# Optimization experiments

Hardware: AMD Instinct MI355X
Metric: run time of the kernel (lower is better)

## Reference

```python
import jax, jax.numpy as jnp
import numpy as np

NEG = float(-2**32 + 1)
LN_EPS = 1e-5

def setup_inputs() -> dict:
    key = jax.random.key(0)
    ks = jax.random.split(key, 10)
    B, Sq, Sk, D = 8, 1024, 1024, 1024
    memory = jax.random.normal(ks[0], (B, Sk, D), jnp.float32)
    decoder_input = jax.random.normal(ks[1], (B, Sq, D), jnp.float32)
    query_mask = jax.random.uniform(ks[2], (B, Sq), jnp.float32)
    Wk = jax.random.normal(ks[3], (D, D), jnp.float32) * 0.02
    Wv = jax.random.normal(ks[4], (D, D), jnp.float32) * 0.02
    Wq = jax.random.normal(ks[5], (D, D), jnp.float32) * 0.02
    Wf = jax.random.normal(ks[6], (2 * D, D), jnp.float32) * 0.02
    bf = jnp.zeros((D,), jnp.float32)
    gamma = jnp.ones((D,), jnp.float32)
    beta = jnp.zeros((D,), jnp.float32)
    mask = jax.random.randint(ks[7], (B, Sq, Sk), 0, 2) == 1
    return dict(memory=memory, decoder_input=decoder_input, query_mask=query_mask,
                Wk=Wk, Wv=Wv, Wq=Wq, Wf=Wf, bf=bf, gamma=gamma, beta=beta, mask=mask)

def reference(memory, decoder_input, query_mask, Wk, Wv, Wq, Wf, bf, gamma, beta, mask):
    B, Sk, D = memory.shape
    Sq = decoder_input.shape[1]
    h = 8
    dh = D // h
    # projections (no bias), split heads -> [h, B, S, dh]
    K = (memory @ Wk).reshape(B, Sk, h, dh).transpose(2, 0, 1, 3)
    V = (memory @ Wv).reshape(B, Sk, h, dh).transpose(2, 0, 1, 3)
    Q = (decoder_input @ Wq).reshape(B, Sq, h, dh).transpose(2, 0, 1, 3)
    # scores [h, B, Sq, Sk]
    attn = jnp.einsum('hbqd,hbkd->hbqk', Q, K) / jnp.sqrt(jnp.float32(dh))
    attn = jnp.where(mask[None], NEG, attn)
    attn = jax.nn.softmax(attn, axis=-1)
    # non-standard post-softmax query-mask multiply
    attn = attn * query_mask[None, :, :, None]
    x = jnp.einsum('hbqk,hbkd->hbqd', attn, V)      # [h,B,Sq,dh]
    x = x.transpose(1, 2, 0, 3).reshape(B, Sq, D)    # concat heads
    x = jnp.concatenate([decoder_input, x], axis=-1)  # [B,Sq,2D]
    x = x @ Wf + bf
    x = x + decoder_input
    # LayerNorm
    mu = jnp.mean(x, axis=-1, keepdims=True)
    var = jnp.var(x, axis=-1, keepdims=True)
    x = (x - mu) * jax.lax.rsqrt(var + LN_EPS) * gamma + beta
    attns = attn.reshape(h * B, Sq, Sk)  # match torch layout [h*B,Sq,Sk]
    return x, attns
```

## Files before the change

### kernel.cpp

```cpp
#include <hip/hip_runtime.h>
#include <hip/hip_bf16.h>
#include <stdint.h>

#define NEG_F (-4294967295.0f)

typedef __attribute__((ext_vector_type(4))) float  floatx4;
typedef __attribute__((ext_vector_type(8))) short  shortx8;

__device__ __forceinline__ unsigned short f2bf(float f) {
    unsigned int u = __builtin_bit_cast(unsigned int, f);
    u += 0x7FFFu + ((u >> 16) & 1u);
    return (unsigned short)(u >> 16);
}

__device__ __forceinline__ uint4 pack8(float4 a, float4 b) {
    uint4 r;
    r.x = (unsigned)f2bf(a.x) | ((unsigned)f2bf(a.y) << 16);
    r.y = (unsigned)f2bf(a.z) | ((unsigned)f2bf(a.w) << 16);
    r.z = (unsigned)f2bf(b.x) | ((unsigned)f2bf(b.y) << 16);
    r.w = (unsigned)f2bf(b.z) | ((unsigned)f2bf(b.w) << 16);
    return r;
}

__global__ __launch_bounds__(256) void cast_bf16(const float* __restrict__ src,
                                                 ushort* __restrict__ dst) {
    long long i = ((long long)blockIdx.x * 256 + threadIdx.x) * 8;
    const float4* p = (const float4*)(src + i);
    float4 f0 = p[0], f1 = p[1];
    *(uint4*)(dst + i) = pack8(f0, f1);
}

__global__ __launch_bounds__(256) void cast_stride(const float* __restrict__ src,
                                                   ushort* __restrict__ dst) {
    long long i = ((long long)blockIdx.x * 256 + threadIdx.x) * 8;
    long long r = i >> 10, c = i & 1023;
    const float4* p = (const float4*)(src + i);
    float4 f0 = p[0], f1 = p[1];
    *(uint4*)(dst + r * 2048 + c) = pack8(f0, f1);
}

__global__ __launch_bounds__(256) void wtrans(const float* __restrict__ W,
                                              ushort* __restrict__ WT, int K, int N) {
    __shared__ float t[32][33];
    int tx = threadIdx.x, ty = threadIdx.y;
    int bx = blockIdx.x * 32;
    int by = blockIdx.y * 32;
    #pragma unroll
    for (int i = 0; i < 4; i++)
        t[ty + 8 * i][tx] = W[(size_t)(by + ty + 8 * i) * N + bx + tx];
    __syncthreads();
    #pragma unroll
    for (int i = 0; i < 4; i++)
        WT[(size_t)(bx + ty + 8 * i) * K + by + tx] = f2bf(t[tx][ty + 8 * i]);
}

__global__ __launch_bounds__(256) void vtrans(const ushort* __restrict__ V,
                                              ushort* __restrict__ VT) {
    __shared__ ushort t[32][33];
    int tx = threadIdx.x, ty = threadIdx.y;
    int bk = blockIdx.x * 32;
    int bd = blockIdx.y * 32;
    int z = blockIdx.z;
    int b = z >> 3, h = z & 7;
    #pragma unroll
    for (int i = 0; i < 4; i++)
        t[ty + 8 * i][tx] = V[((size_t)(b * 1024 + bk + ty + 8 * i)) * 1024 + h * 128 + bd + tx];
    __syncthreads();
    #pragma unroll
    for (int i = 0; i < 4; i++)
        VT[((size_t)((h * 8 + b) * 128 + bd + ty + 8 * i)) * 1024 + bk + tx] = t[tx][ty + 8 * i];
}

template <typename TA, typename TC>
__global__ __launch_bounds__(256) void gemm_bt(
    const TA* __restrict__ A, const ushort* __restrict__ Bt, TC* __restrict__ C,
    int K, int lda, int ldb, int ldc, int zdiv,
    long long sA1, long long sA2, long long sB1, long long sB2,
    long long sC1, long long sC2, float alpha) {
    constexpr int LS = 72;
    __shared__ ushort As[128 * LS];
    __shared__ ushort Bs[128 * LS];

    int z = blockIdx.z;
    int z1 = z / zdiv, z2 = z % zdiv;
    const TA* Ab = A + (long long)z1 * sA1 + (long long)z2 * sA2;
    const ushort* Bb = Bt + (long long)z1 * sB1 + (long long)z2 * sB2;
    TC* Cb = C + (long long)z1 * sC1 + (long long)z2 * sC2;

    int tid = threadIdx.x;
    int bm = blockIdx.y * 128, bn = blockIdx.x * 128;
    int l = tid & 63, wid = tid >> 6;
    int l16 = l & 15, quad = l >> 4;
    int wm = (wid & 1) * 64, wn = (wid >> 1) * 64;

    floatx4 acc[4][4];
    #pragma unroll
    for (int i = 0; i < 4; i++)
        #pragma unroll
        for (int j = 0; j < 4; j++)
            acc[i][j] = {0.0f, 0.0f, 0.0f, 0.0f};

    for (int kt = 0; kt < K; kt += 64) {
        #pragma unroll
        for (int it = 0; it < 4; it++) {
            int lin = it * 256 + tid;
            int row = lin >> 3, col = (lin & 7) << 3;
            uint4 av;
            if constexpr (__is_same(TA, float)) {
                const float4* p = (const float4*)(Ab + (size_t)(bm + row) * lda + kt + col);
                av = pack8(p[0], p[1]);
            } else {
                av = *(const uint4*)(Ab + (size_t)(bm + row) * lda + kt + col);
            }
            *(uint4*)&As[row * LS + col] = av;
            uint4 bv = *(const uint4*)(Bb + (size_t)(bn + row) * ldb + kt + col);
            *(uint4*)&Bs[row * LS + col] = bv;
        }
        __syncthreads();
        #pragma unroll
        for (int kk = 0; kk < 64; kk += 32) {
            shortx8 af[4], bfr[4];
            #pragma unroll
            for (int i = 0; i < 4; i++)
                af[i] = *(const shortx8*)&As[(wm + i * 16 + l16) * LS + kk + quad * 8];
            #pragma unroll
            for (int j = 0; j < 4; j++)
                bfr[j] = *(const shortx8*)&Bs[(wn + j * 16 + l16) * LS + kk + quad * 8];
            #pragma unroll
            for (int i = 0; i < 4; i++)
                #pragma unroll
                for (int j = 0; j < 4; j++)
                    acc[i][j] = __builtin_amdgcn_mfma_f32_16x16x32_bf16(af[i], bfr[j], acc[i][j], 0, 0, 0);
        }
        __syncthreads();
    }

    #pragma unroll
    for (int i = 0; i < 4; i++) {
        #pragma unroll
        for (int j = 0; j < 4; j++) {
            int row0 = bm + wm + i * 16 + quad * 4;
            int col = bn + wn + j * 16 + l16;
            #pragma unroll
            for (int r = 0; r < 4; r++) {
                float v = acc[i][j][r] * alpha;
                size_t idx = (size_t)(row0 + r) * ldc + col;
                if constexpr (__is_same(TC, float)) Cb[idx] = v;
                else Cb[idx] = f2bf(v);
            }
        }
    }
}

__global__ __launch_bounds__(256) void softmax_qm(float* __restrict__ attns,
                                                  const int* __restrict__ mask,
                                                  const float* __restrict__ qmask) {
    __shared__ float sb[4];
    int row = blockIdx.x;
    int hb = row >> 10;
    int b = hb & 7;
    int q = row & 1023;
    float* srow = attns + (size_t)row * 1024;
    const int* mrow = mask + ((size_t)(b * 1024 + q)) * 1024;
    int tid = threadIdx.x;
    int k4 = tid * 4;

    float4 s = *(const float4*)(srow + k4);
    int4 m = *(const int4*)(mrow + k4);
    s.x = m.x ? NEG_F : s.x;
    s.y = m.y ? NEG_F : s.y;
    s.z = m.z ? NEG_F : s.z;
    s.w = m.w ? NEG_F : s.w;

    float mx = fmaxf(fmaxf(s.x, s.y), fmaxf(s.z, s.w));
    #pragma unroll
    for (int o = 32; o; o >>= 1) mx = fmaxf(mx, __shfl_down(mx, o, 64));
    if ((tid & 63) == 0) sb[tid >> 6] = mx;
    __syncthreads();
    mx = fmaxf(fmaxf(sb[0], sb[1]), fmaxf(sb[2], sb[3]));
    __syncthreads();

    float4 p;
    p.x = __expf(s.x - mx);
    p.y = __expf(s.y - mx);
    p.z = __expf(s.z - mx);
    p.w = __expf(s.w - mx);
    float sum = p.x + p.y + p.z + p.w;
    #pragma unroll
    for (int o = 32; o; o >>= 1) sum += __shfl_down(sum, o, 64);
    if ((tid & 63) == 0) sb[tid >> 6] = sum;
    __syncthreads();
    sum = sb[0] + sb[1] + sb[2] + sb[3];

    float scale = qmask[b * 1024 + q] / sum;
    p.x *= scale; p.y *= scale; p.z *= scale; p.w *= scale;
    *(float4*)(srow + k4) = p;
}

__global__ __launch_bounds__(256) void ln_out(const float* __restrict__ ffn,
                                              const float* __restrict__ dec,
                                              const float* __restrict__ bfv,
                                              const float* __restrict__ gamma,
                                              const float* __restrict__ beta,
                                              float* __restrict__ out) {
    __shared__ float sb[8];
    int row = blockIdx.x, tid = threadIdx.x;
    int c = tid * 4;
    size_t base = (size_t)row * 1024 + c;
    float4 x = *(const float4*)(ffn + base);
    float4 d = *(const float4*)(dec + base);
    float4 bb = *(const float4*)(bfv + c);
    x.x += d.x + bb.x; x.y += d.y + bb.y; x.z += d.z + bb.z; x.w += d.w + bb.w;

    float s = x.x + x.y + x.z + x.w;
    float s2 = x.x * x.x + x.y * x.y + x.z * x.z + x.w * x.w;
    #pragma unroll
    for (int o = 32; o; o >>= 1) {
        s += __shfl_down(s, o, 64);
        s2 += __shfl_down(s2, o, 64);
    }
    if ((tid & 63) == 0) { sb[tid >> 6] = s; sb[4 + (tid >> 6)] = s2; }
    __syncthreads();
    s = sb[0] + sb[1] + sb[2] + sb[3];
    s2 = sb[4] + sb[5] + sb[6] + sb[7];
    float mu = s * (1.0f / 1024.0f);
    float var = s2 * (1.0f / 1024.0f) - mu * mu;
    float rs = rsqrtf(var + 1e-5f);

    float4 g = *(const float4*)(gamma + c);
    float4 be = *(const float4*)(beta + c);
    float4 o4;
    o4.x = (x.x - mu) * rs * g.x + be.x;
    o4.y = (x.y - mu) * rs * g.y + be.y;
    o4.z = (x.z - mu) * rs * g.z + be.z;
    o4.w = (x.w - mu) * rs * g.w + be.w;
    *(float4*)(out + base) = o4;
}

extern "C" void kernel_launch(void* const* d_in, const int* in_sizes, int n_in,
                              void* d_out, int out_size, void* d_ws, size_t ws_size,
                              hipStream_t stream) {
    const float* memory  = (const float*)d_in[0];
    const float* decoder = (const float*)d_in[1];
    const float* qmask   = (const float*)d_in[2];
    const float* Wk      = (const float*)d_in[3];
    const float* Wv      = (const float*)d_in[4];
    const float* Wq      = (const float*)d_in[5];
    const float* Wf      = (const float*)d_in[6];
    const float* bfv     = (const float*)d_in[7];
    const float* gamma   = (const float*)d_in[8];
    const float* beta    = (const float*)d_in[9];
    const int*   mask    = (const int*)d_in[10];

    float* xout  = (float*)d_out;
    float* attns = xout + 8388608LL;

    char* w = (char*)d_ws;
    ushort* mem_bf = (ushort*)(w + 0);
    ushort* Kp     = (ushort*)(w + (16LL << 20));
    float*  ffn    = (float*)(w + 0);
    ushort* Qp     = (ushort*)(w + (32LL << 20));
    ushort* Vp     = (ushort*)(w + (48LL << 20));
    ushort* VT     = (ushort*)(w + (64LL << 20));
    ushort* concat = (ushort*)(w + (80LL << 20));
    ushort* WkT    = (ushort*)(w + (112LL << 20));
    ushort* WvT    = (ushort*)(w + (114LL << 20));
    ushort* WqT    = (ushort*)(w + (116LL << 20));
    ushort* WfT    = (ushort*)(w + (118LL << 20));

    const float alpha_s = 0.08838834764831845f;

    cast_bf16<<<4096, 256, 0, stream>>>(memory, mem_bf);
    cast_stride<<<4096, 256, 0, stream>>>(decoder, concat);
    wtrans<<<dim3(32, 32), dim3(32, 8), 0, stream>>>(Wk, WkT, 1024, 1024);
    wtrans<<<dim3(32, 32), dim3(32, 8), 0, stream>>>(Wv, WvT, 1024, 1024);
    wtrans<<<dim3(32, 32), dim3(32, 8), 0, stream>>>(Wq, WqT, 1024, 1024);
    wtrans<<<dim3(32, 64), dim3(32, 8), 0, stream>>>(Wf, WfT, 2048, 1024);
    gemm_bt<ushort, ushort><<<dim3(8, 64, 1), 256, 0, stream>>>(
        mem_bf, WkT, Kp, 1024, 1024, 1024, 1024, 1, 0, 0, 0, 0, 0, 0, 1.0f);
    gemm_bt<ushort, ushort><<<dim3(8, 64, 1), 256, 0, stream>>>(
        mem_bf, WvT, Vp, 1024, 1024, 1024, 1024, 1, 0, 0, 0, 0, 0, 0, 1.0f);
    gemm_bt<ushort, ushort><<<dim3(8, 64, 1), 256, 0, stream>>>(
        concat, WqT, Qp, 1024, 2048, 1024, 1024, 1, 0, 0, 0, 0, 0, 0, 1.0f);
    vtrans<<<dim3(32, 4, 64), dim3(32, 8), 0, stream>>>(Vp, VT);
    gemm_bt<ushort, float><<<dim3(8, 8, 64), 256, 0, stream>>>(
        Qp, Kp, attns, 128, 1024, 1024, 1024, 8,
        128LL, 1048576LL,
        128LL, 1048576LL,
        8388608LL, 1048576LL,
        alpha_s);
    softmax_qm<<<65536, 256, 0, stream>>>(attns, mask, qmask);
    gemm_bt<float, ushort><<<dim3(1, 8, 64), 256, 0, stream>>>(
        attns, VT, concat + 1024, 1024, 1024, 1024, 2048, 8,
        1048576LL, 8388608LL,
        131072LL, 1048576LL,
        2097152LL, 128LL,
        1.0f);
    gemm_bt<ushort, float><<<dim3(8, 64, 1), 256, 0, stream>>>(
        concat, WfT, ffn, 2048, 2048, 2048, 1024, 1, 0, 0, 0, 0, 0, 0, 1.0f);
    ln_out<<<8192, 256, 0, stream>>>(ffn, decoder, bfv, gamma, beta, xout);
}
```

Baseline: 769.0 us.

## Fuse QK scores, masked softmax and PV product into one attention kernel

Replaces the separate QK^T GEMM, softmax kernel and PV GEMM with a single kernel. Each block handles 16 queries of one head, keeps the unnormalized probabilities in LDS as bf16, writes the normalized fp32 attention map once, and multiplies by V^T straight from LDS. This removes several full passes over the large fp32 score tensor in global memory. In exchange, K and V are re-read by every query block, LDS use limits occupancy, and the softmax skips max subtraction and stores probabilities in bf16, which can overflow or lose precision for large scores.

```diff
diff --git a/kernel.cpp b/kernel.cpp
--- a/kernel.cpp
+++ b/kernel.cpp
@@ -1,8 +1,6 @@
 #include <hip/hip_runtime.h>
 #include <hip/hip_bf16.h>
 #include <stdint.h>
-
-#define NEG_F (-4294967295.0f)
 
 typedef __attribute__((ext_vector_type(4))) float  floatx4;
 typedef __attribute__((ext_vector_type(8))) short  shortx8;
@@ -11,6 +9,10 @@
     unsigned int u = __builtin_bit_cast(unsigned int, f);
     u += 0x7FFFu + ((u >> 16) & 1u);
     return (unsigned short)(u >> 16);
+}
+__device__ __forceinline__ float bf2f(unsigned short h) {
+    unsigned int u = (unsigned int)h << 16;
+    return __builtin_bit_cast(float, u);
 }
 
 __device__ __forceinline__ uint4 pack8(float4 a, float4 b) {
@@ -71,21 +73,13 @@
         VT[((size_t)((h * 8 + b) * 128 + bd + ty + 8 * i)) * 1024 + bk + tx] = t[tx][ty + 8 * i];
 }
 
-template <typename TA, typename TC>
+template <typename TC>
 __global__ __launch_bounds__(256) void gemm_bt(
-    const TA* __restrict__ A, const ushort* __restrict__ Bt, TC* __restrict__ C,
-    int K, int lda, int ldb, int ldc, int zdiv,
-    long long sA1, long long sA2, long long sB1, long long sB2,
-    long long sC1, long long sC2, float alpha) {
+    const ushort* __restrict__ A, const ushort* __restrict__ Bt, TC* __restrict__ C,
+    int K, int lda, int ldb, int ldc) {
     constexpr int LS = 72;
     __shared__ ushort As[128 * LS];
     __shared__ ushort Bs[128 * LS];
-
-    int z = blockIdx.z;
-    int z1 = z / zdiv, z2 = z % zdiv;
-    const TA* Ab = A + (long long)z1 * sA1 + (long long)z2 * sA2;
-    const ushort* Bb = Bt + (long long)z1 * sB1 + (long long)z2 * sB2;
-    TC* Cb = C + (long long)z1 * sC1 + (long long)z2 * sC2;
 
     int tid = threadIdx.x;
     int bm = blockIdx.y * 128, bn = blockIdx.x * 128;
@@ -105,15 +99,9 @@
         for (int it = 0; it < 4; it++) {
             int lin = it * 256 + tid;
             int row = lin >> 3, col = (lin & 7) << 3;
-            uint4 av;
-            if constexpr (__is_same(TA, float)) {
-                const float4* p = (const float4*)(Ab + (size_t)(bm + row) * lda + kt + col);
-                av = pack8(p[0], p[1]);
-            } else {
-                av = *(const uint4*)(Ab + (size_t)(bm + row) * lda + kt + col);
-            }
+            uint4 av = *(const uint4*)(A + (size_t)(bm + row) * lda + kt + col);
             *(uint4*)&As[row * LS + col] = av;
-            uint4 bv = *(const uint4*)(Bb + (size_t)(bn + row) * ldb + kt + col);
+            uint4 bv = *(const uint4*)(Bt + (size_t)(bn + row) * ldb + kt + col);
             *(uint4*)&Bs[row * LS + col] = bv;
         }
         __syncthreads();
@@ -143,58 +131,140 @@
             int col = bn + wn + j * 16 + l16;
             #pragma unroll
             for (int r = 0; r < 4; r++) {
-                float v = acc[i][j][r] * alpha;
+                float v = acc[i][j][r];
                 size_t idx = (size_t)(row0 + r) * ldc + col;
-                if constexpr (__is_same(TC, float)) Cb[idx] = v;
-                else Cb[idx] = f2bf(v);
+                if constexpr (__is_same(TC, float)) C[idx] = v;
+                else C[idx] = f2bf(v);
             }
         }
     }
 }
 
-__global__ __launch_bounds__(256) void softmax_qm(float* __restrict__ attns,
-                                                  const int* __restrict__ mask,
-                                                  const float* __restrict__ qmask) {
-    __shared__ float sb[4];
-    int row = blockIdx.x;
-    int hb = row >> 10;
-    int b = hb & 7;
-    int q = row & 1023;
-    float* srow = attns + (size_t)row * 1024;
-    const int* mrow = mask + ((size_t)(b * 1024 + q)) * 1024;
-    int tid = threadIdx.x;
-    int k4 = tid * 4;
-
-    float4 s = *(const float4*)(srow + k4);
-    int4 m = *(const int4*)(mrow + k4);
-    s.x = m.x ? NEG_F : s.x;
-    s.y = m.y ? NEG_F : s.y;
-    s.z = m.z ? NEG_F : s.z;
-    s.w = m.w ? NEG_F : s.w;
-
-    float mx = fmaxf(fmaxf(s.x, s.y), fmaxf(s.z, s.w));
-    #pragma unroll
-    for (int o = 32; o; o >>= 1) mx = fmaxf(mx, __shfl_down(mx, o, 64));
-    if ((tid & 63) == 0) sb[tid >> 6] = mx;
-    __syncthreads();
-    mx = fmaxf(fmaxf(sb[0], sb[1]), fmaxf(sb[2], sb[3]));
-    __syncthreads();
-
-    float4 p;
-    p.x = __expf(s.x - mx);
-    p.y = __expf(s.y - mx);
-    p.z = __expf(s.z - mx);
-    p.w = __expf(s.w - mx);
-    float sum = p.x + p.y + p.z + p.w;
-    #pragma unroll
-    for (int o = 32; o; o >>= 1) sum += __shfl_down(sum, o, 64);
-    if ((tid & 63) == 0) sb[tid >> 6] = sum;
-    __syncthreads();
-    sum = sb[0] + sb[1] + sb[2] + sb[3];
-
-    float scale = qmask[b * 1024 + q] / sum;
-    p.x *= scale; p.y *= scale; p.z *= scale; p.w *= scale;
-    *(float4*)(srow + k4) = p;
+__global__ __launch_bounds__(256) void fused_attn(
+    const ushort* __restrict__ Qp, const ushort* __restrict__ Kp,
+    const ushort* __restrict__ VT, const int* __restrict__ mask,
+    const float* __restrict__ qmask, float* __restrict__ attns,
+    ushort* __restrict__ concat) {
+    __shared__ ushort Qs[16 * 136];
+    __shared__ ushort Kv[4 * 2304];
+    __shared__ ushort Ss[16 * 1032];
+    __shared__ float rowpart[16][17];
+    __shared__ float scale_s[16];
+
+    const int b = blockIdx.z, h = blockIdx.y, q0 = blockIdx.x * 16;
+    const int tid = threadIdx.x;
+    const int w = tid >> 6, l = tid & 63;
+    const int l16 = l & 15, quad = l >> 4;
+    const float sc = 0.08838834764831845f;
+
+    {
+        int row = tid >> 4, col = (tid & 15) * 8;
+        *(uint4*)&Qs[row * 136 + col] =
+            *(const uint4*)(Qp + (size_t)(b * 1024 + q0 + row) * 1024 + h * 128 + col);
+    }
+    __syncthreads();
+
+    shortx8 af[4];
+    #pragma unroll
+    for (int kk = 0; kk < 4; kk++)
+        af[kk] = *(const shortx8*)&Qs[l16 * 136 + kk * 32 + quad * 8];
+
+    ushort* Ksw = &Kv[w * 2304];
+    const size_t mbase = (size_t)b * 1048576 + (size_t)q0 * 1024;
+    for (int c = 0; c < 16; ++c) {
+        int k0 = c * 64 + w * 16;
+        #pragma unroll
+        for (int i = 0; i < 4; ++i) {
+            int lin = i * 64 + l;
+            int kr = lin >> 4, col = (lin & 15) * 8;
+            *(uint4*)&Ksw[kr * 136 + col] =
+                *(const uint4*)(Kp + (size_t)(b * 1024 + k0 + kr) * 1024 + h * 128 + col);
+        }
+        floatx4 acc = {0.0f, 0.0f, 0.0f, 0.0f};
+        #pragma unroll
+        for (int kk = 0; kk < 4; ++kk) {
+            shortx8 bfr = *(const shortx8*)&Ksw[l16 * 136 + kk * 32 + quad * 8];
+            acc = __builtin_amdgcn_mfma_f32_16x16x32_bf16(af[kk], bfr, acc, 0, 0, 0);
+        }
+        #pragma unroll
+        for (int r = 0; r < 4; ++r) {
+            int q = quad * 4 + r;
+            int m = mask[mbase + (size_t)q * 1024 + k0 + l16];
+            float v = m ? 0.0f : __expf(acc[r] * sc);
+            Ss[q * 1032 + k0 + l16] = f2bf(v);
+        }
+    }
+    __syncthreads();
+
+    {
+        int row = tid >> 4, cs = (tid & 15) * 64;
+        float s = 0.0f;
+        #pragma unroll
+        for (int i = 0; i < 8; ++i) {
+            shortx8 v = *(const shortx8*)&Ss[row * 1032 + cs + i * 8];
+            #pragma unroll
+            for (int j = 0; j < 8; ++j) s += bf2f((unsigned short)v[j]);
+        }
+        rowpart[row][tid & 15] = s;
+    }
+    __syncthreads();
+    if (tid < 16) {
+        float s = 0.0f;
+        #pragma unroll
+        for (int i = 0; i < 16; ++i) s += rowpart[tid][i];
+        scale_s[tid] = qmask[b * 1024 + q0 + tid] / s;
+    }
+    __syncthreads();
+
+    {
+        int row = tid >> 4;
+        float scl = scale_s[row];
+        float* arow = attns + ((size_t)((h * 8 + b) * 1024 + q0 + row)) * 1024;
+        int c0 = (tid & 15) * 4;
+        #pragma unroll
+        for (int j = 0; j < 16; ++j) {
+            int c = c0 + j * 64;
+            ushort4 v = *(const ushort4*)&Ss[row * 1032 + c];
+            float4 o;
+            o.x = bf2f(v.x) * scl;
+            o.y = bf2f(v.y) * scl;
+            o.z = bf2f(v.z) * scl;
+            o.w = bf2f(v.w) * scl;
+            *(float4*)(arow + c) = o;
+        }
+    }
+
+    ushort* Vsw = &Kv[w * 2304];
+    const ushort* Vb = VT + (size_t)((h * 8 + b) * 128 + w * 32) * 1024;
+    floatx4 oacc[2] = {{0.0f, 0.0f, 0.0f, 0.0f}, {0.0f, 0.0f, 0.0f, 0.0f}};
+    for (int c = 0; c < 16; ++c) {
+        #pragma unroll
+        for (int i = 0; i < 4; ++i) {
+            int lin = i * 64 + l;
+            int dr = lin >> 3, ko = (lin & 7) * 8;
+            *(uint4*)&Vsw[dr * 72 + ko] =
+                *(const uint4*)(Vb + (size_t)dr * 1024 + c * 64 + ko);
+        }
+        #pragma unroll
+        for (int ks = 0; ks < 2; ++ks) {
+            shortx8 a = *(const shortx8*)&Ss[l16 * 1032 + c * 64 + ks * 32 + quad * 8];
+            #pragma unroll
+            for (int j = 0; j < 2; ++j) {
+                shortx8 bfr = *(const shortx8*)&Vsw[(j * 16 + l16) * 72 + ks * 32 + quad * 8];
+                oacc[j] = __builtin_amdgcn_mfma_f32_16x16x32_bf16(a, bfr, oacc[j], 0, 0, 0);
+            }
+        }
+    }
+    #pragma unroll
+    for (int j = 0; j < 2; ++j) {
+        #pragma unroll
+        for (int r = 0; r < 4; ++r) {
+            int q = quad * 4 + r;
+            int d = w * 32 + j * 16 + l16;
+            float v = oacc[j][r] * scale_s[q];
+            concat[(size_t)(b * 1024 + q0 + q) * 2048 + 1024 + h * 128 + d] = f2bf(v);
+        }
+    }
 }
 
 __global__ __launch_bounds__(256) void ln_out(const float* __restrict__ ffn,
@@ -268,35 +338,17 @@
     ushort* WqT    = (ushort*)(w + (116LL << 20));
     ushort* WfT    = (ushort*)(w + (118LL << 20));
 
-    const float alpha_s = 0.08838834764831845f;
-
     cast_bf16<<<4096, 256, 0, stream>>>(memory, mem_bf);
     cast_stride<<<4096, 256, 0, stream>>>(decoder, concat);
     wtrans<<<dim3(32, 32), dim3(32, 8), 0, stream>>>(Wk, WkT, 1024, 1024);
     wtrans<<<dim3(32, 32), dim3(32, 8), 0, stream>>>(Wv, WvT, 1024, 1024);
     wtrans<<<dim3(32, 32), dim3(32, 8), 0, stream>>>(Wq, WqT, 1024, 1024);
     wtrans<<<dim3(32, 64), dim3(32, 8), 0, stream>>>(Wf, WfT, 2048, 1024);
-    gemm_bt<ushort, ushort><<<dim3(8, 64, 1), 256, 0, stream>>>(
-        mem_bf, WkT, Kp, 1024, 1024, 1024, 1024, 1, 0, 0, 0, 0, 0, 0, 1.0f);
-    gemm_bt<ushort, ushort><<<dim3(8, 64, 1), 256, 0, stream>>>(
-        mem_bf, WvT, Vp, 1024, 1024, 1024, 1024, 1, 0, 0, 0, 0, 0, 0, 1.0f);
-    gemm_bt<ushort, ushort><<<dim3(8, 64, 1), 256, 0, stream>>>(
-        concat, WqT, Qp, 1024, 2048, 1024, 1024, 1, 0, 0, 0, 0, 0, 0, 1.0f);
+    gemm_bt<ushort><<<dim3(8, 64), 256, 0, stream>>>(mem_bf, WkT, Kp, 1024, 1024, 1024, 1024);
+    gemm_bt<ushort><<<dim3(8, 64), 256, 0, stream>>>(mem_bf, WvT, Vp, 1024, 1024, 1024, 1024);
+    gemm_bt<ushort><<<dim3(8, 64), 256, 0, stream>>>(concat, WqT, Qp, 1024, 2048, 1024, 1024);
     vtrans<<<dim3(32, 4, 64), dim3(32, 8), 0, stream>>>(Vp, VT);
-    gemm_bt<ushort, float><<<dim3(8, 8, 64), 256, 0, stream>>>(
-        Qp, Kp, attns, 128, 1024, 1024, 1024, 8,
-        128LL, 1048576LL,
-        128LL, 1048576LL,
-        8388608LL, 1048576LL,
-        alpha_s);
-    softmax_qm<<<65536, 256, 0, stream>>>(attns, mask, qmask);
-    gemm_bt<float, ushort><<<dim3(1, 8, 64), 256, 0, stream>>>(
-        attns, VT, concat + 1024, 1024, 1024, 1024, 2048, 8,
-        1048576LL, 8388608LL,
-        131072LL, 1048576LL,
-        2097152LL, 128LL,
-        1.0f);
-    gemm_bt<ushort, float><<<dim3(8, 64, 1), 256, 0, stream>>>(
-        concat, WfT, ffn, 2048, 2048, 2048, 1024, 1, 0, 0, 0, 0, 0, 0, 1.0f);
+    fused_attn<<<dim3(64, 8, 8), 256, 0, stream>>>(Qp, Kp, VT, mask, qmask, attns, concat);
+    gemm_bt<float><<<dim3(8, 64), 256, 0, stream>>>(concat, WfT, ffn, 2048, 2048, 2048, 1024);
     ln_out<<<8192, 256, 0, stream>>>(ffn, decoder, bfv, gamma, beta, xout);
 }
```

Result: faster. 708.0 us (-7.9%).
